# Kernel tuning notes

Measured on AMD Instinct MI355X. Metric: run time of the kernel, lower is better.

Reference implementation:

```python
import jax, jax.numpy as jnp
import numpy as np
from jax import lax

WINDOW_SIZE = 11
SIGMA = 1.5
C1 = 0.01 ** 2
C2 = 0.03 ** 2


def _gaussian_window(channels: int) -> jnp.ndarray:
    x = np.arange(WINDOW_SIZE)
    g = np.exp(-((x - WINDOW_SIZE // 2) ** 2) / (2.0 * SIGMA ** 2))
    g = g / g.sum()
    w2d = np.outer(g, g).astype(np.float32)  # [k,k]
    # depthwise kernel: [C, 1, k, k] in OIHW with feature_group_count=C
    return jnp.asarray(np.tile(w2d[None, None], (channels, 1, 1, 1)))


def _depthwise_blur(x: jnp.ndarray, window: jnp.ndarray) -> jnp.ndarray:
    pad = WINDOW_SIZE // 2
    return lax.conv_general_dilated(
        x, window,
        window_strides=(1, 1),
        padding=[(pad, pad), (pad, pad)],
        feature_group_count=x.shape[1],
        dimension_numbers=("NCHW", "OIHW", "NCHW"),
    )


def setup_inputs() -> dict:
    key = jax.random.key(0)
    k1, k2 = jax.random.split(key)
    pred = jax.random.normal(k1, (16, 3, 512, 512), dtype=jnp.float32)
    target = jax.random.normal(k2, (16, 3, 512, 512), dtype=jnp.float32)
    return {"pred": pred, "target": target}


def reference(pred, target):
    pred = (pred + 1.0) / 2.0
    target = (target + 1.0) / 2.0
    channels = pred.shape[1]
    window = _gaussian_window(channels)

    mu_p = _depthwise_blur(pred, window)
    mu_t = _depthwise_blur(target, window)
    mu_p_sq = mu_p * mu_p
    mu_t_sq = mu_t * mu_t
    mu_pt = mu_p * mu_t

    sigma_p_sq = _depthwise_blur(pred * pred, window) - mu_p_sq
    sigma_t_sq = _depthwise_blur(target * target, window) - mu_t_sq
    sigma_pt = _depthwise_blur(pred * target, window) - mu_pt

    ssim_map = ((2.0 * mu_pt + C1) * (2.0 * sigma_pt + C2)) / (
        (mu_p_sq + mu_t_sq + C1) * (sigma_p_sq + sigma_t_sq + C2)
    )
    return 1.0 - jnp.mean(ssim_map)
```

## Files before the change

### kernel.cpp

```cpp
#include <hip/hip_runtime.h>
#include <math.h>


#define IMG 512
#define TW 64
#define TH 16
#define GXD 8
#define GYD 32
#define GZD 48
#define NB (GXD * GYD * GZD)
#define VBS 88
#define C1c 0.0001f
#define C2c 0.0009f
#define NTOTAL 12582912.0f

typedef short bf16x8 __attribute__((ext_vector_type(8)));
typedef float f32x4 __attribute__((ext_vector_type(4)));

struct GaussB { unsigned short gb[11]; };

__device__ __forceinline__ unsigned int pkbf(float a, float b) {
    return __builtin_amdgcn_perm(__float_as_uint(b), __float_as_uint(a),
                                 0x07060302u);
}

template <bool USE_ATOMIC>
__global__ __launch_bounds__(256, 8) void ssim_main(
    const float* __restrict__ pred,
    const float* __restrict__ target,
    float* __restrict__ sink,
    GaussB gwb)
{
    __shared__ unsigned short Wmat[16][32];
    __shared__ unsigned short vb[5][16][VBS];
    __shared__ float red[4];

    const int tid  = threadIdx.x;
    const int w    = tid >> 6;
    const int lane = tid & 63;
    const int quad = lane >> 4;
    const int n16  = lane & 15;
    const int tx0  = blockIdx.x * TW;
    const int ty0  = blockIdx.y * TH;
    const float* __restrict__ pbase = pred   + (size_t)blockIdx.z * (IMG * IMG);
    const float* __restrict__ tbase = target + (size_t)blockIdx.z * (IMG * IMG);

    for (int idx = tid; idx < 512; idx += 256) {
        int i = idx >> 5, k = idx & 31, d = k - i;
        Wmat[i][k] = (d >= 0 && d <= 10) ? gwb.gb[d] : 0;
    }
    __syncthreads();

    const bf16x8 wfrag = *(const bf16x8*)&Wmat[n16][quad * 8];

    const bool interior = (blockIdx.x >= 1) & (blockIdx.x <= GXD - 2) &
                          (blockIdx.y >= 1) & (blockIdx.y <= GYD - 2);
    const f32x4 z = {0.0f, 0.0f, 0.0f, 0.0f};

    for (int vc = w; vc < 5; vc += 4) {
        const int gx = tx0 - 5 + 16 * vc + n16;
        const int k0 = quad * 8;
        float pv[8], tv[8];
        if (interior) {
            const float* pp = pbase + (size_t)(ty0 - 5 + k0) * IMG + gx;
            const float* tp = tbase + (size_t)(ty0 - 5 + k0) * IMG + gx;
            #pragma unroll
            for (int j = 0; j < 8; ++j) {
                pv[j] = pp[j * IMG];
                tv[j] = tp[j * IMG];
            }
        } else {
            const bool xin = (unsigned)gx < (unsigned)IMG;
            #pragma unroll
            for (int j = 0; j < 8; ++j) {
                int gy = ty0 - 5 + k0 + j;
                bool in = xin && ((unsigned)gy < (unsigned)IMG);
                int idx = in ? (gy * IMG + gx) : 0;
                float a = pbase[idx];
                float b = tbase[idx];
                pv[j] = in ? a : 0.0f;
                tv[j] = in ? b : 0.0f;
            }
        }
        union { bf16x8 v; unsigned int u[4]; } fP, fT, fPP, fTT, fPT;
        #pragma unroll
        for (int h = 0; h < 4; ++h) {
            float p0 = fmaf(pv[2*h],   0.5f, 0.5f);
            float p1 = fmaf(pv[2*h+1], 0.5f, 0.5f);
            float t0 = fmaf(tv[2*h],   0.5f, 0.5f);
            float t1 = fmaf(tv[2*h+1], 0.5f, 0.5f);
            fP.u[h]  = pkbf(p0, p1);
            fT.u[h]  = pkbf(t0, t1);
            fPP.u[h] = pkbf(p0 * p0, p1 * p1);
            fTT.u[h] = pkbf(t0 * t0, t1 * t1);
            fPT.u[h] = pkbf(p0 * t0, p1 * t1);
        }
        f32x4 d0 = __builtin_amdgcn_mfma_f32_16x16x32_bf16(fP.v,  wfrag, z, 0, 0, 0);
        f32x4 d1 = __builtin_amdgcn_mfma_f32_16x16x32_bf16(fT.v,  wfrag, z, 0, 0, 0);
        f32x4 d2 = __builtin_amdgcn_mfma_f32_16x16x32_bf16(fPP.v, wfrag, z, 0, 0, 0);
        f32x4 d3 = __builtin_amdgcn_mfma_f32_16x16x32_bf16(fTT.v, wfrag, z, 0, 0, 0);
        f32x4 d4 = __builtin_amdgcn_mfma_f32_16x16x32_bf16(fPT.v, wfrag, z, 0, 0, 0);
        const int vcol = 16 * vc + 4 * quad;
        {
            union { ushort4 s; unsigned int u[2]; } pk;
            pk.u[0] = pkbf(d0[0], d0[1]); pk.u[1] = pkbf(d0[2], d0[3]);
            *(ushort4*)&vb[0][n16][vcol] = pk.s;
            pk.u[0] = pkbf(d1[0], d1[1]); pk.u[1] = pkbf(d1[2], d1[3]);
            *(ushort4*)&vb[1][n16][vcol] = pk.s;
            pk.u[0] = pkbf(d2[0], d2[1]); pk.u[1] = pkbf(d2[2], d2[3]);
            *(ushort4*)&vb[2][n16][vcol] = pk.s;
            pk.u[0] = pkbf(d3[0], d3[1]); pk.u[1] = pkbf(d3[2], d3[3]);
            *(ushort4*)&vb[3][n16][vcol] = pk.s;
            pk.u[0] = pkbf(d4[0], d4[1]); pk.u[1] = pkbf(d4[2], d4[3]);
            *(ushort4*)&vb[4][n16][vcol] = pk.s;
        }
    }
    __syncthreads();

    f32x4 r[5];
    #pragma unroll
    for (int ch = 0; ch < 5; ++ch) {
        bf16x8 a = *(const bf16x8*)&vb[ch][n16][16 * w + 8 * quad];
        r[ch] = __builtin_amdgcn_mfma_f32_16x16x32_bf16(a, wfrag, z, 0, 0, 0);
    }

    float lsum = 0.0f;
    #pragma unroll
    for (int j = 0; j < 4; ++j) {
        float mp = r[0][j], mt = r[1][j];
        float mp2 = mp * mp, mt2 = mt * mt, mpt = mp * mt;
        float sig_p  = r[2][j] - mp2;
        float sig_t  = r[3][j] - mt2;
        float sig_pt = r[4][j] - mpt;
        float num = (2.0f * mpt + C1c) * (2.0f * sig_pt + C2c);
        float den = (mp2 + mt2 + C1c) * (sig_p + sig_t + C2c);
        lsum = fmaf(num, __builtin_amdgcn_rcpf(den), lsum);
    }

    #pragma unroll
    for (int off = 32; off > 0; off >>= 1)
        lsum += __shfl_down(lsum, off, 64);
    if (lane == 0) red[w] = lsum;
    __syncthreads();
    if (tid == 0) {
        float s = red[0] + red[1] + red[2] + red[3];
        if (USE_ATOMIC) {
            atomicAdd(sink, s);
        } else {
            int bid = blockIdx.x + GXD * (blockIdx.y + GYD * blockIdx.z);
            sink[bid] = s;
        }
    }
}

__global__ __launch_bounds__(256) void ssim_reduce(const float* __restrict__ partials,
                                                   float* __restrict__ out)
{
    __shared__ float red[4];
    const int tid = threadIdx.x;
    float s = 0.0f;
    const float4* p4 = (const float4*)partials;
    #pragma unroll
    for (int j = 0; j < NB / 1024; ++j) {
        float4 v = p4[tid + 256 * j];
        s += v.x + v.y + v.z + v.w;
    }
    #pragma unroll
    for (int off = 32; off > 0; off >>= 1)
        s += __shfl_down(s, off, 64);
    if ((tid & 63) == 0) red[tid >> 6] = s;
    __syncthreads();
    if (tid == 0)
        out[0] = 1.0f - (red[0] + red[1] + red[2] + red[3]) / NTOTAL;
}

__global__ void ssim_zero(float* accum) { accum[0] = 0.0f; }
__global__ void ssim_final(const float* accum, float* out) {
    out[0] = 1.0f - accum[0] / NTOTAL;
}

extern "C" void kernel_launch(void* const* d_in, const int* in_sizes, int n_in,
                              void* d_out, int out_size, void* d_ws, size_t ws_size,
                              hipStream_t stream) {
    const float* pred   = (const float*)d_in[0];
    const float* target = (const float*)d_in[1];
    float* out = (float*)d_out;

    GaussB gwb;
    double vals[11], s = 0.0;
    for (int i = 0; i < 11; ++i) {
        double d = (double)i - 5.0;
        vals[i] = exp(-(d * d) / (2.0 * 1.5 * 1.5));
        s += vals[i];
    }
    for (int i = 0; i < 11; ++i) {
        float f = (float)(vals[i] / s);
        unsigned int u;
        __builtin_memcpy(&u, &f, 4);
        unsigned int rounded = (u + 0x7FFFu + ((u >> 16) & 1u)) >> 16;
        gwb.gb[i] = (unsigned short)rounded;
    }

    dim3 grid(GXD, GYD, GZD);
    if (ws_size >= (size_t)NB * sizeof(float)) {
        float* partials = (float*)d_ws;
        ssim_main<false><<<grid, 256, 0, stream>>>(pred, target, partials, gwb);
        ssim_reduce<<<1, 256, 0, stream>>>(partials, out);
    } else {
        float* accum = (float*)d_ws;
        ssim_zero<<<1, 1, 0, stream>>>(accum);
        ssim_main<true><<<grid, 256, 0, stream>>>(pred, target, accum, gwb);
        ssim_final<<<1, 1, 0, stream>>>(accum, out);
    }
}
```

Baseline: 137.5 us.

## Process four row tiles per block with register prefetch and a fifth wave

Each block now walks four vertically stacked 16-row tiles, so the grid shrinks in y. While one tile is being computed, the next tile's input columns are loaded into a double-buffered register set. A fifth wave is added so that all five 16-column vertical-pass strips run in parallel, instead of wave 0 doing two. A barrier that waits only on LDS operations lets the prefetched global loads stay in flight across the synchronisation. The aim is to hide global-load latency and balance work across waves. In exchange, registers per thread and the per-block serial chain grow, which may reduce occupancy or parallelism.

```diff
diff --git a/kernel.cpp b/kernel.cpp
--- a/kernel.cpp
+++ b/kernel.cpp
@@ -5,8 +5,9 @@
 #define IMG 512
 #define TW 64
 #define TH 16
+#define NT 4
 #define GXD 8
-#define GYD 32
+#define GYD 8
 #define GZD 48
 #define NB (GXD * GYD * GZD)
 #define VBS 88
@@ -24,8 +25,41 @@
                                  0x07060302u);
 }
 
+__device__ __forceinline__ void barrier_lds_only() {
+    __builtin_amdgcn_s_waitcnt(0xc07f);
+    __builtin_amdgcn_s_barrier();
+}
+
+__device__ __forceinline__ void load_col8(const float* __restrict__ pbase,
+                                          const float* __restrict__ tbase,
+                                          int gx, int gy0, bool xin,
+                                          float* pv, float* tv)
+{
+    const bool ok = xin & (gy0 >= 0) & (gy0 <= IMG - 8);
+    if (ok) {
+        const float* pp = pbase + gy0 * IMG + gx;
+        const float* tp = tbase + gy0 * IMG + gx;
+        #pragma unroll
+        for (int j = 0; j < 8; ++j) {
+            pv[j] = pp[j * IMG];
+            tv[j] = tp[j * IMG];
+        }
+    } else {
+        #pragma unroll
+        for (int j = 0; j < 8; ++j) {
+            int gy = gy0 + j;
+            bool in = xin && ((unsigned)gy < (unsigned)IMG);
+            int idx = in ? (gy * IMG + gx) : 0;
+            float a = pbase[idx];
+            float b = tbase[idx];
+            pv[j] = in ? a : 0.0f;
+            tv[j] = in ? b : 0.0f;
+        }
+    }
+}
+
 template <bool USE_ATOMIC>
-__global__ __launch_bounds__(256, 8) void ssim_main(
+__global__ __launch_bounds__(320, 8) void ssim_main(
     const float* __restrict__ pred,
     const float* __restrict__ target,
     float* __restrict__ sink,
@@ -33,7 +67,7 @@
 {
     __shared__ unsigned short Wmat[16][32];
     __shared__ unsigned short vb[5][16][VBS];
-    __shared__ float red[4];
+    __shared__ float red[5];
 
     const int tid  = threadIdx.x;
     const int w    = tid >> 6;
@@ -41,100 +75,82 @@
     const int quad = lane >> 4;
     const int n16  = lane & 15;
     const int tx0  = blockIdx.x * TW;
-    const int ty0  = blockIdx.y * TH;
+    const int tyb  = blockIdx.y * (TH * NT);
     const float* __restrict__ pbase = pred   + (size_t)blockIdx.z * (IMG * IMG);
     const float* __restrict__ tbase = target + (size_t)blockIdx.z * (IMG * IMG);
 
-    for (int idx = tid; idx < 512; idx += 256) {
+    for (int idx = tid; idx < 512; idx += 320) {
         int i = idx >> 5, k = idx & 31, d = k - i;
         Wmat[i][k] = (d >= 0 && d <= 10) ? gwb.gb[d] : 0;
     }
     __syncthreads();
-
     const bf16x8 wfrag = *(const bf16x8*)&Wmat[n16][quad * 8];
 
-    const bool interior = (blockIdx.x >= 1) & (blockIdx.x <= GXD - 2) &
-                          (blockIdx.y >= 1) & (blockIdx.y <= GYD - 2);
+    const int gx  = tx0 - 5 + 16 * w + n16;
+    const bool xin = (unsigned)gx < (unsigned)IMG;
+    const int k0  = quad * 8;
+    const int vcol = 16 * w + 4 * quad;
     const f32x4 z = {0.0f, 0.0f, 0.0f, 0.0f};
 
-    for (int vc = w; vc < 5; vc += 4) {
-        const int gx = tx0 - 5 + 16 * vc + n16;
-        const int k0 = quad * 8;
-        float pv[8], tv[8];
-        if (interior) {
-            const float* pp = pbase + (size_t)(ty0 - 5 + k0) * IMG + gx;
-            const float* tp = tbase + (size_t)(ty0 - 5 + k0) * IMG + gx;
+    float pv[2][8], tv[2][8];
+    load_col8(pbase, tbase, gx, tyb - 5 + k0, xin, pv[0], tv[0]);
+
+    float lsum = 0.0f;
+
+    #pragma unroll
+    for (int i = 0; i < NT; ++i) {
+        const int cur = i & 1, nxt = cur ^ 1;
+        if (i + 1 < NT)
+            load_col8(pbase, tbase, gx, tyb + TH * (i + 1) - 5 + k0, xin,
+                      pv[nxt], tv[nxt]);
+
+        float ps[8], ts[8];
+        #pragma unroll
+        for (int j = 0; j < 8; ++j) {
+            ps[j] = fmaf(pv[cur][j], 0.5f, 0.5f);
+            ts[j] = fmaf(tv[cur][j], 0.5f, 0.5f);
+        }
+        #pragma unroll
+        for (int ch = 0; ch < 5; ++ch) {
+            union { bf16x8 v; unsigned int u[4]; } f;
             #pragma unroll
-            for (int j = 0; j < 8; ++j) {
-                pv[j] = pp[j * IMG];
-                tv[j] = tp[j * IMG];
+            for (int h = 0; h < 4; ++h) {
+                float a0, a1;
+                if      (ch == 0) { a0 = ps[2*h];            a1 = ps[2*h+1]; }
+                else if (ch == 1) { a0 = ts[2*h];            a1 = ts[2*h+1]; }
+                else if (ch == 2) { a0 = ps[2*h]*ps[2*h];    a1 = ps[2*h+1]*ps[2*h+1]; }
+                else if (ch == 3) { a0 = ts[2*h]*ts[2*h];    a1 = ts[2*h+1]*ts[2*h+1]; }
+                else              { a0 = ps[2*h]*ts[2*h];    a1 = ps[2*h+1]*ts[2*h+1]; }
+                f.u[h] = pkbf(a0, a1);
             }
-        } else {
-            const bool xin = (unsigned)gx < (unsigned)IMG;
+            f32x4 d = __builtin_amdgcn_mfma_f32_16x16x32_bf16(f.v, wfrag, z, 0, 0, 0);
+            union { ushort4 s; unsigned int u[2]; } pk;
+            pk.u[0] = pkbf(d[0], d[1]);
+            pk.u[1] = pkbf(d[2], d[3]);
+            *(ushort4*)&vb[ch][n16][vcol] = pk.s;
+        }
+        barrier_lds_only();
+
+        if (w < 4) {
+            f32x4 r[5];
             #pragma unroll
-            for (int j = 0; j < 8; ++j) {
-                int gy = ty0 - 5 + k0 + j;
-                bool in = xin && ((unsigned)gy < (unsigned)IMG);
-                int idx = in ? (gy * IMG + gx) : 0;
-                float a = pbase[idx];
-                float b = tbase[idx];
-                pv[j] = in ? a : 0.0f;
-                tv[j] = in ? b : 0.0f;
+            for (int ch = 0; ch < 5; ++ch) {
+                bf16x8 a = *(const bf16x8*)&vb[ch][n16][16 * w + 8 * quad];
+                r[ch] = __builtin_amdgcn_mfma_f32_16x16x32_bf16(a, wfrag, z, 0, 0, 0);
             }
-        }
-        union { bf16x8 v; unsigned int u[4]; } fP, fT, fPP, fTT, fPT;
-        #pragma unroll
-        for (int h = 0; h < 4; ++h) {
-            float p0 = fmaf(pv[2*h],   0.5f, 0.5f);
-            float p1 = fmaf(pv[2*h+1], 0.5f, 0.5f);
-            float t0 = fmaf(tv[2*h],   0.5f, 0.5f);
-            float t1 = fmaf(tv[2*h+1], 0.5f, 0.5f);
-            fP.u[h]  = pkbf(p0, p1);
-            fT.u[h]  = pkbf(t0, t1);
-            fPP.u[h] = pkbf(p0 * p0, p1 * p1);
-            fTT.u[h] = pkbf(t0 * t0, t1 * t1);
-            fPT.u[h] = pkbf(p0 * t0, p1 * t1);
-        }
-        f32x4 d0 = __builtin_amdgcn_mfma_f32_16x16x32_bf16(fP.v,  wfrag, z, 0, 0, 0);
-        f32x4 d1 = __builtin_amdgcn_mfma_f32_16x16x32_bf16(fT.v,  wfrag, z, 0, 0, 0);
-        f32x4 d2 = __builtin_amdgcn_mfma_f32_16x16x32_bf16(fPP.v, wfrag, z, 0, 0, 0);
-        f32x4 d3 = __builtin_amdgcn_mfma_f32_16x16x32_bf16(fTT.v, wfrag, z, 0, 0, 0);
-        f32x4 d4 = __builtin_amdgcn_mfma_f32_16x16x32_bf16(fPT.v, wfrag, z, 0, 0, 0);
-        const int vcol = 16 * vc + 4 * quad;
-        {
-            union { ushort4 s; unsigned int u[2]; } pk;
-            pk.u[0] = pkbf(d0[0], d0[1]); pk.u[1] = pkbf(d0[2], d0[3]);
-            *(ushort4*)&vb[0][n16][vcol] = pk.s;
-            pk.u[0] = pkbf(d1[0], d1[1]); pk.u[1] = pkbf(d1[2], d1[3]);
-            *(ushort4*)&vb[1][n16][vcol] = pk.s;
-            pk.u[0] = pkbf(d2[0], d2[1]); pk.u[1] = pkbf(d2[2], d2[3]);
-            *(ushort4*)&vb[2][n16][vcol] = pk.s;
-            pk.u[0] = pkbf(d3[0], d3[1]); pk.u[1] = pkbf(d3[2], d3[3]);
-            *(ushort4*)&vb[3][n16][vcol] = pk.s;
-            pk.u[0] = pkbf(d4[0], d4[1]); pk.u[1] = pkbf(d4[2], d4[3]);
-            *(ushort4*)&vb[4][n16][vcol] = pk.s;
-        }
-    }
-    __syncthreads();
-
-    f32x4 r[5];
-    #pragma unroll
-    for (int ch = 0; ch < 5; ++ch) {
-        bf16x8 a = *(const bf16x8*)&vb[ch][n16][16 * w + 8 * quad];
-        r[ch] = __builtin_amdgcn_mfma_f32_16x16x32_bf16(a, wfrag, z, 0, 0, 0);
-    }
-
-    float lsum = 0.0f;
-    #pragma unroll
-    for (int j = 0; j < 4; ++j) {
-        float mp = r[0][j], mt = r[1][j];
-        float mp2 = mp * mp, mt2 = mt * mt, mpt = mp * mt;
-        float sig_p  = r[2][j] - mp2;
-        float sig_t  = r[3][j] - mt2;
-        float sig_pt = r[4][j] - mpt;
-        float num = (2.0f * mpt + C1c) * (2.0f * sig_pt + C2c);
-        float den = (mp2 + mt2 + C1c) * (sig_p + sig_t + C2c);
-        lsum = fmaf(num, __builtin_amdgcn_rcpf(den), lsum);
+            #pragma unroll
+            for (int j = 0; j < 4; ++j) {
+                float mp = r[0][j], mt = r[1][j];
+                float mp2 = mp * mp, mt2 = mt * mt, mpt = mp * mt;
+                float sig_p  = r[2][j] - mp2;
+                float sig_t  = r[3][j] - mt2;
+                float sig_pt = r[4][j] - mpt;
+                float num = (2.0f * mpt + C1c) * (2.0f * sig_pt + C2c);
+                float den = (mp2 + mt2 + C1c) * (sig_p + sig_t + C2c);
+                lsum = fmaf(num, __builtin_amdgcn_rcpf(den), lsum);
+            }
+        }
+        __syncthreads();
     }
 
     #pragma unroll
@@ -204,12 +220,12 @@
     dim3 grid(GXD, GYD, GZD);
     if (ws_size >= (size_t)NB * sizeof(float)) {
         float* partials = (float*)d_ws;
-        ssim_main<false><<<grid, 256, 0, stream>>>(pred, target, partials, gwb);
+        ssim_main<false><<<grid, 320, 0, stream>>>(pred, target, partials, gwb);
         ssim_reduce<<<1, 256, 0, stream>>>(partials, out);
     } else {
         float* accum = (float*)d_ws;
         ssim_zero<<<1, 1, 0, stream>>>(accum);
-        ssim_main<true><<<grid, 256, 0, stream>>>(pred, target, accum, gwb);
+        ssim_main<true><<<grid, 320, 0, stream>>>(pred, target, accum, gwb);
         ssim_final<<<1, 1, 0, stream>>>(accum, out);
     }
 }
```

After: 159.7 us. 16.1% more time.
